# Kernel tuning notes

Measured on AMD Instinct MI355X. Metric: run time of the kernel, lower is better.

The kernel has to match this reference:

```python
import jax, jax.numpy as jnp
import numpy as np


def _ccl(x, w, b):
    # FFT-domain circular conv: rfft2 -> complex multiply + sum over c_in -> irfft2 + bias
    H, W = x.shape[-2], x.shape[-1]
    xf = jnp.fft.rfft2(x)                 # [B, Ci, H, Wf] complex
    wf = jnp.fft.rfft2(w, s=(H, W))       # [Co, Ci, H, Wf] complex
    hf = jnp.einsum('bihw,oihw->bohw', xf, wf)
    return jnp.fft.irfft2(hf, s=(H, W)) + b[:, None, None]


def _maxpool(x, ph, pw):
    B, C, H, W = x.shape
    return x.reshape(B, C, H // ph, ph, W // pw, pw).max(axis=(3, 5))


def _upsample_zero(x, sh, sw):
    B, C, H, W = x.shape
    y = jnp.zeros((B, C, H * sh, W * sw), dtype=x.dtype)
    return y.at[:, :, ::sh, ::sw].set(x)


def setup_inputs() -> dict:
    key = jax.random.key(0)
    ks = jax.random.split(key, 11)
    inp = {"x": jax.random.normal(ks[0], (16, 2, 64, 256), dtype=jnp.float32)}
    specs = [  # (c_out, c_in, kh, kw)
        (50, 1, 3, 7), (50, 50, 3, 7), (50, 50, 3, 5), (50, 50, 3, 7), (1, 50, 3, 7)]
    for i, (co, ci, kh, kw) in enumerate(specs):
        K = float(np.sqrt(1.0 / (ci * kh * kw)))
        inp[f"w{i+1}"] = (2 * jax.random.uniform(ks[2 * i + 1], (co, ci, kh, kw), dtype=jnp.float32) - 1) * K
        inp[f"b{i+1}"] = (2 * jax.random.uniform(ks[2 * i + 2], (co,), dtype=jnp.float32) - 1) * K
    return inp


def reference(x, w1, b1, w2, b2, w3, b3, w4, b4, w5, b5):
    H, W = x.shape[-2], x.shape[-1]
    h = x.reshape(-1, 1, H, W)                       # [2B, 1, 64, 256]
    h = jax.nn.relu(_maxpool(_ccl(h, w1, b1), 2, 4))  # [2B, 50, 32, 64]
    h = jax.nn.relu(_maxpool(_ccl(h, w2, b2), 2, 4))  # [2B, 50, 16, 16]
    h = h.reshape(-1, 2, h.shape[-3], h.shape[-2], h.shape[-1])
    h = h[:, 0] + h[:, 1].mean(axis=(-1, -2))[..., None, None]  # [B, 50, 16, 16]
    h = jax.nn.relu(_ccl(_upsample_zero(h, 2, 4), w3, b3))       # [B, 50, 32, 64]
    h = jax.nn.relu(_ccl(_upsample_zero(h, 2, 4), w4, b4))       # [B, 50, 64, 256]
    h = jax.nn.sigmoid(_ccl(h, w5, b5))                          # [B, 1, 64, 256]
    return h.squeeze(1)
```

## Files before the change

kernel.cpp:

```cpp
#include <hip/hip_runtime.h>
#include <math.h>

__global__ void kprep(const float* __restrict__ w2, const float* __restrict__ w3,
                      const float* __restrict__ w4, float* __restrict__ w2t,
                      float* __restrict__ w3t, float* __restrict__ w4t) {
  int i = blockIdx.x * 256 + threadIdx.x;
  if (i < 52500) {
    int co = i % 50, r = i / 50;
    w2t[i] = w2[co * 1050 + r];
    w4t[i] = w4[co * 1050 + r];
  } else {
    int j = i - 52500;
    if (j < 37500) {
      int co = j % 50, r = j / 50;
      w3t[j] = w3[co * 750 + r];
    }
  }
}

__global__ __launch_bounds__(256) void k1(const float* __restrict__ x,
                                          const float* __restrict__ w1,
                                          const float* __restrict__ b1,
                                          float* __restrict__ a1) {
  int b = blockIdx.z;
  int pr0 = blockIdx.x * 4;
  int co0 = blockIdx.y * 10;
  int ty = threadIdx.x >> 6;
  int pc = threadIdx.x & 63;
  int pr = pr0 + ty;
  const float* xb = x + b * (64 * 256);
  float xw[4][10];
#pragma unroll
  for (int r = 0; r < 4; ++r) {
    int row = (2 * pr - 2 + r) & 63;
#pragma unroll
    for (int c = 0; c < 10; ++c) {
      int col = (4 * pc - 6 + c) & 255;
      xw[r][c] = xb[row * 256 + col];
    }
  }
#pragma unroll
  for (int cq = 0; cq < 10; ++cq) {
    int co = co0 + cq;
    const float* wp = w1 + co * 21;
    float m = -1e30f;
#pragma unroll
    for (int iy = 0; iy < 2; ++iy) {
#pragma unroll
      for (int jx = 0; jx < 4; ++jx) {
        float s = 0.f;
#pragma unroll
        for (int di = 0; di < 3; ++di)
#pragma unroll
          for (int dj = 0; dj < 7; ++dj)
            s = fmaf(xw[iy + 2 - di][jx + 6 - dj], wp[di * 7 + dj], s);
        m = fmaxf(m, s);
      }
    }
    float v = fmaxf(m + b1[co], 0.f);
    a1[((b * 50 + co) * 32 + pr) * 64 + pc] = v;
  }
}

__global__ __launch_bounds__(256) void k2(const float* __restrict__ a1,
                                          const float* __restrict__ w2t,
                                          const float* __restrict__ b2,
                                          float* __restrict__ a2) {
  __shared__ __align__(16) float sm[3840];
  int b = blockIdx.z;
  int r0 = blockIdx.x * 4;
  int co0 = blockIdx.y * 10;
  int y = threadIdx.x >> 6;
  int xcol = threadIdx.x & 63;
  const float* p[7];
#pragma unroll
  for (int dj = 0; dj < 7; ++dj) p[dj] = sm + y * 64 + ((xcol - dj) & 63);
  float acc[10];
#pragma unroll
  for (int co = 0; co < 10; ++co) acc[co] = b2[co0 + co];
  const float* ain = a1 + b * (50 * 2048);
  for (int cci = 0; cci < 5; ++cci) {
    __syncthreads();
    for (int e = threadIdx.x; e < 960; e += 256) {
      int ci = e / 96;
      int rem = e - ci * 96;
      int rr = rem >> 4;
      int c4 = rem & 15;
      int row = (r0 - 2 + rr) & 31;
      *(float4*)&sm[(ci * 6 + rr) * 64 + c4 * 4] =
          *(const float4*)&ain[(cci * 10 + ci) * 2048 + row * 64 + c4 * 4];
    }
    __syncthreads();
    const float* q0 = p[0]; const float* q1 = p[1]; const float* q2 = p[2];
    const float* q3 = p[3]; const float* q4 = p[4]; const float* q5 = p[5];
    const float* q6 = p[6];
    for (int ci = 0; ci < 10; ++ci) {
      const float* wci = w2t + (cci * 10 + ci) * 1050 + co0;
#pragma unroll
      for (int di = 0; di < 3; ++di) {
        const int ro = (2 - di) * 64;
        float xv0 = q0[ro], xv1 = q1[ro], xv2 = q2[ro], xv3 = q3[ro];
        float xv4 = q4[ro], xv5 = q5[ro], xv6 = q6[ro];
        const float* wr = wci + di * 7 * 50;
#pragma unroll
        for (int co = 0; co < 10; ++co) acc[co] = fmaf(xv0, wr[co], acc[co]);
#pragma unroll
        for (int co = 0; co < 10; ++co) acc[co] = fmaf(xv1, wr[50 + co], acc[co]);
#pragma unroll
        for (int co = 0; co < 10; ++co) acc[co] = fmaf(xv2, wr[100 + co], acc[co]);
#pragma unroll
        for (int co = 0; co < 10; ++co) acc[co] = fmaf(xv3, wr[150 + co], acc[co]);
#pragma unroll
        for (int co = 0; co < 10; ++co) acc[co] = fmaf(xv4, wr[200 + co], acc[co]);
#pragma unroll
        for (int co = 0; co < 10; ++co) acc[co] = fmaf(xv5, wr[250 + co], acc[co]);
#pragma unroll
        for (int co = 0; co < 10; ++co) acc[co] = fmaf(xv6, wr[300 + co], acc[co]);
      }
      q0 += 384; q1 += 384; q2 += 384; q3 += 384; q4 += 384; q5 += 384; q6 += 384;
    }
  }
  __syncthreads();
#pragma unroll
  for (int k = 0; k < 10; ++k)
    sm[k * 256 + y * 64 + xcol] = acc[k];
  __syncthreads();
  for (int w = threadIdx.x; w < 320; w += 256) {
    int cop = w / 32;
    int pr = (w >> 4) & 1;
    int pc = w & 15;
    float m = -1e30f;
#pragma unroll
    for (int yy = 0; yy < 2; ++yy)
#pragma unroll
      for (int xx = 0; xx < 4; ++xx)
        m = fmaxf(m, sm[cop * 256 + (pr * 2 + yy) * 64 + pc * 4 + xx]);
    m = fmaxf(m, 0.f);
    a2[((b * 50 + co0 + cop) * 16 + (r0 >> 1) + pr) * 16 + pc] = m;
  }
}

__global__ __launch_bounds__(512) void k3(const float* __restrict__ a2,
                                          const float* __restrict__ w3t,
                                          const float* __restrict__ b3,
                                          float* __restrict__ a3) {
  __shared__ float ts[4000];
  __shared__ float mean_s[64];
  __shared__ float part[200];
  int b = blockIdx.z;
  int r0 = blockIdx.x * 8;
  int co0 = blockIdx.y * 10;
  int tid = threadIdx.x;
  const float* aodd = a2 + (2 * b + 1) * (50 * 256);
  if (tid < 200) {
    int ci = tid >> 2, p = tid & 3;
    float s = 0.f;
    for (int k = 0; k < 64; ++k) s += aodd[ci * 256 + p * 64 + k];
    part[tid] = s;
  }
  __syncthreads();
  if (tid < 50)
    mean_s[tid] = (part[4 * tid] + part[4 * tid + 1] + part[4 * tid + 2] + part[4 * tid + 3]) * (1.f / 256.f);
  __syncthreads();
  const float* aev = a2 + (2 * b) * (50 * 256);
  for (int e = tid; e < 4000; e += 512) {
    int ci = e / 80;
    int rr = (e >> 4) % 5;
    int tc = e & 15;
    int trow = ((r0 >> 1) - 1 + rr) & 15;
    ts[e] = aev[ci * 256 + trow * 16 + tc] + mean_s[ci];
  }
  __syncthreads();
  int wv = __builtin_amdgcn_readfirstlane(tid >> 6);
  int lane = tid & 63;
  int p = wv >> 2;
  int m = wv & 3;
  int q = lane & 15;
  int yidx = lane >> 4;
  int i = r0 + 2 * yidx + p;
  int j = 4 * q + m;
  float acc[10];
#pragma unroll
  for (int co = 0; co < 10; ++co) acc[co] = b3[co0 + co];
  int ndi = (p == 0) ? 2 : 1;
  int ndj = (m == 0) ? 2 : 1;
  for (int aa = 0; aa < ndi; ++aa) {
    int di = (p == 0) ? (2 * aa) : 1;
    int rr = 1 + ((2 * yidx + p - di) >> 1);
    for (int e2 = 0; e2 < ndj; ++e2) {
      int dj = (m == 0) ? (4 * e2) : m;
      int tc = ((j - dj + 64) >> 2) & 15;
      for (int ci = 0; ci < 50; ++ci) {
        float xv = ts[ci * 80 + rr * 16 + tc];
        const float* wrow = w3t + (ci * 15 + di * 5 + dj) * 50 + co0;
#pragma unroll
        for (int co = 0; co < 10; ++co)
          acc[co] = fmaf(xv, wrow[co], acc[co]);
      }
    }
  }
  float* aout = a3 + b * (50 * 2048);
#pragma unroll
  for (int co = 0; co < 10; ++co)
    aout[(co0 + co) * 2048 + i * 64 + j] = fmaxf(acc[co], 0.f);
}

__global__ __launch_bounds__(512) void k4(const float* __restrict__ a3,
                                          const float* __restrict__ w4t,
                                          const float* __restrict__ b4,
                                          float* __restrict__ a4) {
  __shared__ float s4[6400];
  int b = blockIdx.z;
  int r0 = blockIdx.x * 2;
  int co0 = blockIdx.y * 10;
  int tid = threadIdx.x;
  const float* ain = a3 + b * (50 * 2048);
  for (int e = tid; e < 6400; e += 512) {
    int ci = e >> 7;
    int rr = (e >> 6) & 1;
    int col = e & 63;
    int row = ((r0 >> 1) - 1 + rr) & 31;
    s4[e] = ain[ci * 2048 + row * 64 + col];
  }
  __syncthreads();
  int wv = __builtin_amdgcn_readfirstlane(tid >> 6);
  int lane = tid & 63;
  int rowsel = wv >> 2;
  int m = wv & 3;
  int i = r0 + rowsel;
  int j = 4 * lane + m;
  float acc[10];
#pragma unroll
  for (int co = 0; co < 10; ++co) acc[co] = b4[co0 + co];
  int ndi = (rowsel == 0) ? 2 : 1;
  int ndj = (m < 3) ? 2 : 1;
  for (int aa = 0; aa < ndi; ++aa) {
    int di = (rowsel == 0) ? (2 * aa) : 1;
    int rr = 1 - (di >> 1);
    for (int e2 = 0; e2 < ndj; ++e2) {
      int dj = m + 4 * e2;
      int tc = ((j - dj) >> 2) & 63;
      for (int ci = 0; ci < 50; ++ci) {
        float xv = s4[ci * 128 + rr * 64 + tc];
        const float* wrow = w4t + (ci * 21 + di * 7 + dj) * 50 + co0;
#pragma unroll
        for (int co = 0; co < 10; ++co)
          acc[co] = fmaf(xv, wrow[co], acc[co]);
      }
    }
  }
  float* aout = a4 + b * (50 * 16384);
#pragma unroll
  for (int co = 0; co < 10; ++co)
    aout[(co0 + co) * 16384 + i * 256 + j] = fmaxf(acc[co], 0.f);
}

__global__ __launch_bounds__(256) void k5(const float* __restrict__ a4,
                                          const float* __restrict__ w5,
                                          const float* __restrict__ b5,
                                          float* __restrict__ out) {
  __shared__ __align__(16) float s5[7920];
  int bid = blockIdx.x;
  int b = bid >> 4;
  int r0 = (bid & 15) * 4;
  int tid = threadIdx.x;
  int y = tid >> 6;
  int q = tid & 63;
  int j0 = q * 4;
  float acc0 = b5[0], acc1 = b5[0], acc2 = b5[0], acc3 = b5[0];
  const float* ain = a4 + b * (50 * 16384);
  for (int cc = 0; cc < 10; ++cc) {
    __syncthreads();
    for (int e = tid; e < 7920; e += 256) {
      int ci = e / 1584;
      int rr = (e / 264) % 6;
      int c = e % 264;
      int row = (r0 - 2 + rr) & 63;
      int col = (c - 8) & 255;
      s5[e] = ain[(cc * 5 + ci) * 16384 + row * 256 + col];
    }
    __syncthreads();
#pragma unroll
    for (int ci = 0; ci < 5; ++ci) {
#pragma unroll
      for (int di = 0; di < 3; ++di) {
        const float4* prow = (const float4*)&s5[ci * 1584 + (y + 2 - di) * 264 + j0];
        float4 v0 = prow[0], v1 = prow[1], v2 = prow[2];
        float wnd[12] = {v0.x, v0.y, v0.z, v0.w, v1.x, v1.y, v1.z, v1.w,
                         v2.x, v2.y, v2.z, v2.w};
        const float* wp = w5 + ((cc * 5 + ci) * 3 + di) * 7;
#pragma unroll
        for (int dj = 0; dj < 7; ++dj) {
          float wgt = wp[dj];
          acc0 = fmaf(wnd[8 - dj], wgt, acc0);
          acc1 = fmaf(wnd[9 - dj], wgt, acc1);
          acc2 = fmaf(wnd[10 - dj], wgt, acc2);
          acc3 = fmaf(wnd[11 - dj], wgt, acc3);
        }
      }
    }
  }
  float4 r;
  r.x = 1.f / (1.f + expf(-acc0));
  r.y = 1.f / (1.f + expf(-acc1));
  r.z = 1.f / (1.f + expf(-acc2));
  r.w = 1.f / (1.f + expf(-acc3));
  *(float4*)(out + b * 16384 + (r0 + y) * 256 + j0) = r;
}

extern "C" void kernel_launch(void* const* d_in, const int* in_sizes, int n_in,
                              void* d_out, int out_size, void* d_ws, size_t ws_size,
                              hipStream_t stream) {
  (void)in_sizes; (void)n_in; (void)out_size; (void)ws_size;
  const float* x  = (const float*)d_in[0];
  const float* w1 = (const float*)d_in[1];
  const float* b1 = (const float*)d_in[2];
  const float* w2 = (const float*)d_in[3];
  const float* b2 = (const float*)d_in[4];
  const float* w3 = (const float*)d_in[5];
  const float* b3 = (const float*)d_in[6];
  const float* w4 = (const float*)d_in[7];
  const float* b4 = (const float*)d_in[8];
  const float* w5 = (const float*)d_in[9];
  const float* b5 = (const float*)d_in[10];
  float* out = (float*)d_out;
  float* ws  = (float*)d_ws;
  float* w2t = ws;
  float* w3t = w2t + 52500;
  float* w4t = w3t + 37500;
  float* a1  = w4t + 52500;
  float* a2  = a1 + 32 * 50 * 32 * 64;
  float* a3  = a2 + 32 * 50 * 16 * 16;
  float* a4  = a3 + 16 * 50 * 32 * 64;
  hipLaunchKernelGGL(kprep, dim3(352), dim3(256), 0, stream, w2, w3, w4, w2t, w3t, w4t);
  hipLaunchKernelGGL(k1, dim3(8, 5, 32), dim3(256), 0, stream, x, w1, b1, a1);
  hipLaunchKernelGGL(k2, dim3(8, 5, 32), dim3(256), 0, stream, a1, w2t, b2, a2);
  hipLaunchKernelGGL(k3, dim3(4, 5, 16), dim3(512), 0, stream, a2, w3t, b3, a3);
  hipLaunchKernelGGL(k4, dim3(32, 5, 16), dim3(512), 0, stream, a3, w4t, b4, a4);
  hipLaunchKernelGGL(k5, dim3(256), dim3(256), 0, stream, a4, w5, b5, out);
}
```

Before: 353.3 us.

## Double-buffer k2 input tiles with direct global-to-LDS async loads

Kernel k2 now stages input channel chunks into two LDS buffers, issuing the load for the next chunk of ten channels before computing on the current one. It also uses the AMD global_load_lds builtin so the data goes straight from global memory into LDS without passing through registers. The aim is to hide global load latency behind the FMA loop and remove one barrier per chunk. The cost is doubled LDS use (about 30KB), which may lower occupancy. The code also relies on the wave-uniform LDS base layout of global_load_lds and on the barrier waiting for those loads to finish.

```diff
diff --git a/kernel.cpp b/kernel.cpp
--- a/kernel.cpp
+++ b/kernel.cpp
@@ -1,5 +1,10 @@
 #include <hip/hip_runtime.h>
 #include <math.h>
+
+__device__ __forceinline__ void gload_lds16(const float* g, float* l) {
+  __builtin_amdgcn_global_load_lds((const __attribute__((address_space(1))) void*)g,
+                                   (__attribute__((address_space(3))) void*)l, 16, 0, 0);
+}
 
 __global__ void kprep(const float* __restrict__ w2, const float* __restrict__ w3,
                       const float* __restrict__ w4, float* __restrict__ w2t,
@@ -66,34 +71,61 @@
                                           const float* __restrict__ w2t,
                                           const float* __restrict__ b2,
                                           float* __restrict__ a2) {
-  __shared__ __align__(16) float sm[3840];
+  __shared__ __align__(16) float sm[7680];
   int b = blockIdx.z;
   int r0 = blockIdx.x * 4;
   int co0 = blockIdx.y * 10;
-  int y = threadIdx.x >> 6;
-  int xcol = threadIdx.x & 63;
-  const float* p[7];
-#pragma unroll
-  for (int dj = 0; dj < 7; ++dj) p[dj] = sm + y * 64 + ((xcol - dj) & 63);
+  int tid = threadIdx.x;
+  int y = tid >> 6;
+  int xcol = tid & 63;
+  int off[7];
+#pragma unroll
+  for (int dj = 0; dj < 7; ++dj) off[dj] = y * 64 + ((xcol - dj) & 63);
   float acc[10];
 #pragma unroll
   for (int co = 0; co < 10; ++co) acc[co] = b2[co0 + co];
   const float* ain = a1 + b * (50 * 2048);
-  for (int cci = 0; cci < 5; ++cci) {
-    __syncthreads();
-    for (int e = threadIdx.x; e < 960; e += 256) {
-      int ci = e / 96;
-      int rem = e - ci * 96;
+  int wbase = tid & 192;
+
+#pragma unroll
+  for (int k = 0; k < 4; ++k) {
+    int gb = k * 256 + wbase;
+    if (gb < 960) {
+      int g = gb + xcol;
+      int ci = g / 96;
+      int rem = g - ci * 96;
       int rr = rem >> 4;
       int c4 = rem & 15;
       int row = (r0 - 2 + rr) & 31;
-      *(float4*)&sm[(ci * 6 + rr) * 64 + c4 * 4] =
-          *(const float4*)&ain[(cci * 10 + ci) * 2048 + row * 64 + c4 * 4];
-    }
-    __syncthreads();
-    const float* q0 = p[0]; const float* q1 = p[1]; const float* q2 = p[2];
-    const float* q3 = p[3]; const float* q4 = p[4]; const float* q5 = p[5];
-    const float* q6 = p[6];
+      gload_lds16(ain + ci * 2048 + row * 64 + c4 * 4, sm + gb * 4);
+    }
+  }
+  __syncthreads();
+
+  for (int cci = 0; cci < 5; ++cci) {
+    int cur = cci & 1;
+    if (cci < 4) {
+      float* dst = sm + (cur ^ 1) * 3840;
+#pragma unroll
+      for (int k = 0; k < 4; ++k) {
+        int gb = k * 256 + wbase;
+        if (gb < 960) {
+          int g = gb + xcol;
+          int ci = g / 96;
+          int rem = g - ci * 96;
+          int rr = rem >> 4;
+          int c4 = rem & 15;
+          int row = (r0 - 2 + rr) & 31;
+          gload_lds16(ain + ((cci + 1) * 10 + ci) * 2048 + row * 64 + c4 * 4,
+                      dst + gb * 4);
+        }
+      }
+    }
+    const float* cb = sm + cur * 3840;
+    const float* q0 = cb + off[0]; const float* q1 = cb + off[1];
+    const float* q2 = cb + off[2]; const float* q3 = cb + off[3];
+    const float* q4 = cb + off[4]; const float* q5 = cb + off[5];
+    const float* q6 = cb + off[6];
     for (int ci = 0; ci < 10; ++ci) {
       const float* wci = w2t + (cci * 10 + ci) * 1050 + co0;
 #pragma unroll
@@ -119,8 +151,8 @@
       }
       q0 += 384; q1 += 384; q2 += 384; q3 += 384; q4 += 384; q5 += 384; q6 += 384;
     }
-  }
-  __syncthreads();
+    __syncthreads();
+  }
 #pragma unroll
   for (int k = 0; k < 10; ++k)
     sm[k * 256 + y * 64 + xcol] = acc[k];
```

Result: no change. 350.0 us (-1.0%).
